# Optimization experiments

Hardware: AMD Instinct MI355X
Metric: run time of the kernel (lower is better)

## Reference

```python
import jax, jax.numpy as jnp
import numpy as np


def setup_inputs() -> dict:
    key = jax.random.key(0)
    k0, k1, k2, k3, k4 = jax.random.split(key, 5)
    B, S, D, E, H = 2, 4096, 1024, 8, 512
    x = jax.random.normal(k0, (B, S, D), jnp.float32)
    w_router = jax.random.normal(k1, (D, E), jnp.float32) * (D ** -0.5)
    w1 = jax.random.normal(k2, (E, D, H), jnp.float32) * (D ** -0.5)
    w2 = jax.random.normal(k3, (E, H, D), jnp.float32) * (H ** -0.5)
    w3 = jax.random.normal(k4, (E, D, H), jnp.float32) * (D ** -0.5)
    return {"x": x, "w_router": w_router, "w1": w1, "w2": w2, "w3": w3, "top_k": 2}


def reference(x, w_router, w1, w2, w3, top_k):
    """MoE layer: linear router -> softmax -> top_k, then grouped SwiGLU experts
    combined with the routing weights. out = sum_k w_k * Expert_{idx_k}(x)."""
    B, S, D = x.shape
    E = w_router.shape[1]
    xt = x.reshape(-1, D)                              # [T, D]
    T = xt.shape[0]

    # Router
    logits = xt @ w_router                             # [T, E]
    probs = jax.nn.softmax(logits, axis=-1)
    weights, idx = jax.lax.top_k(probs, top_k)         # [T, k], [T, k]

    # Scatter top-k weights into a dense per-token gate over experts.
    gate = jnp.zeros((T, E), xt.dtype).at[jnp.arange(T)[:, None], idx].add(weights)

    h = jax.nn.silu(jnp.einsum('td,edh->teh', xt, w1)) * jnp.einsum('td,edh->teh', xt, w3)
    y = jnp.einsum('te,teh,ehd->td', gate, h, w2)      # combine
    return y.reshape(B, S, D)
```

## Files before the change

kernel.cpp:

```cpp
#include <hip/hip_runtime.h>

#define NT    8192
#define DIM   1024
#define NE    8
#define NH    512
#define NROWS (NT*2)

typedef _Float16 f16;
typedef unsigned int u32;
typedef __attribute__((ext_vector_type(8))) _Float16 f16x8;
typedef __attribute__((ext_vector_type(4))) _Float16 f16x4;
typedef __attribute__((ext_vector_type(2))) _Float16 f16x2;
typedef __attribute__((ext_vector_type(4))) float f32x4;

__device__ __forceinline__ void gl2lds16(const f16* gptr, f16* ldsptr) {
    __builtin_amdgcn_global_load_lds(
        (const __attribute__((address_space(1))) u32*)gptr,
        (__attribute__((address_space(3))) u32*)ldsptr, 16, 0, 0);
}

#define FR(sbuf, row, q) \
    (*(const f16x8*)&sbuf[(row)*32 + (((q) ^ (((row) >> 1) & 3)) << 3)])

#define KC 512
__global__ __launch_bounds__(256) void prep_kernel(
    const float* __restrict__ x, const float* __restrict__ wr,
    const float* __restrict__ w1, const float* __restrict__ w3,
    const float* __restrict__ w2, float* __restrict__ plogits,
    f16* __restrict__ x16,
    f16* __restrict__ w1t, f16* __restrict__ w3t, f16* __restrict__ w2t,
    int* __restrict__ zint)
{
    __shared__ float smem[NE*KC];
    int tid = threadIdx.x;
    int bi = blockIdx.x;
    if (bi == 0 && tid < 16) zint[tid] = 0;
    if (bi < 1024) {
        int bx = bi & 511, by = bi >> 9;
        int kc0 = by * KC;
        for (int i = tid; i < NE*KC; i += 256) {
            int k = i >> 3, e = i & 7;
            smem[e*KC + k] = wr[(size_t)kc0*NE + i];
        }
        __syncthreads();
        int tok = bx*16 + (tid >> 4);
        int kl  = tid & 15;
        float acc[NE];
        #pragma unroll
        for (int e = 0; e < NE; e++) acc[e] = 0.f;
        const float* xrow = x + (size_t)tok*DIM + kc0;
        f16* xhrow = x16 + (size_t)tok*DIM + kc0;
        #pragma unroll
        for (int i = 0; i < KC/64; i++) {
            int kb = i*64 + kl*4;
            float4 xv = *(const float4*)(xrow + kb);
            f16x4 xh = { (f16)xv.x, (f16)xv.y, (f16)xv.z, (f16)xv.w };
            *(f16x4*)(xhrow + kb) = xh;
            #pragma unroll
            for (int e = 0; e < NE; e++) {
                float4 wv = *(const float4*)&smem[e*KC + kb];
                acc[e] += xv.x*wv.x + xv.y*wv.y + xv.z*wv.z + xv.w*wv.w;
            }
        }
        #pragma unroll
        for (int e = 0; e < NE; e++) {
            float v = acc[e];
            v += __shfl_xor(v, 1); v += __shfl_xor(v, 2);
            v += __shfl_xor(v, 4); v += __shfl_xor(v, 8);
            acc[e] = v;
        }
        if (kl == 0) {
            float* pp = plogits + ((size_t)by*NT + tok)*NE;
            float4 o0 = {acc[0], acc[1], acc[2], acc[3]};
            float4 o1 = {acc[4], acc[5], acc[6], acc[7]};
            *(float4*)pp = o0;
            *(float4*)(pp + 4) = o1;
        }
    } else {
        int tz = bi - 1024;
        int zx = tz & 127, zy = tz >> 7;
        int tensor = zy >> 3, e = zy & 7;
        const float* src; f16* dst; int R, C;
        if (tensor == 0)      { src = w1; dst = w1t; R = DIM; C = NH; }
        else if (tensor == 1) { src = w3; dst = w3t; R = DIM; C = NH; }
        else                  { src = w2; dst = w2t; R = NH; C = DIM; }
        src += (size_t)e * DIM * NH;
        dst += (size_t)e * DIM * NH;
        int tcols = C >> 6;
        int bx = zx % tcols, by = zx / tcols;
        int r0 = by*64, c0 = bx*64;
        #pragma unroll
        for (int p = 0; p < 4; p++) {
            int r = p*16 + (tid >> 4);
            int c = (tid & 15) << 2;
            float4 v = *(const float4*)&src[(size_t)(r0 + r)*C + c0 + c];
            *(float4*)&smem[r*64 + (c ^ (((r >> 3) & 7) << 2))] = v;
        }
        __syncthreads();
        #pragma unroll
        for (int pass = 0; pass < 2; pass++) {
            int s = pass*256 + tid;
            int h = s >> 3, a = s & 7, d0 = a << 3;
            int hs = h ^ (a << 2);
            f16x8 o;
            #pragma unroll
            for (int j = 0; j < 8; j++)
                o[j] = (f16)smem[(d0 + j)*64 + hs];
            *(f16x8*)&dst[(size_t)(c0 + h)*R + r0 + d0] = o;
        }
    }
}

__global__ __launch_bounds__(256) void route_kernel(
    const float* __restrict__ plogits, unsigned char* __restrict__ ge,
    float* __restrict__ gw, int* __restrict__ zint)
{
    __shared__ int lhist[NE];
    int tid = threadIdx.x;
    if (tid < NE) lhist[tid] = 0;
    __syncthreads();

    int t = blockIdx.x*256 + tid;
    const float* p0 = plogits + (size_t)t*NE;
    const float* p1 = plogits + (size_t)NT*NE + (size_t)t*NE;
    float4 a0 = *(const float4*)p0, a1 = *(const float4*)(p0+4);
    float4 b0 = *(const float4*)p1, b1 = *(const float4*)(p1+4);
    float l[NE] = { a0.x+b0.x, a0.y+b0.y, a0.z+b0.z, a0.w+b0.w,
                    a1.x+b1.x, a1.y+b1.y, a1.z+b1.z, a1.w+b1.w };
    float m = l[0];
    #pragma unroll
    for (int e = 1; e < NE; e++) m = fmaxf(m, l[e]);
    float s = 0.f;
    #pragma unroll
    for (int e = 0; e < NE; e++) { l[e] = __expf(l[e] - m); s += l[e]; }
    float inv = 1.f / s;
    int i0 = 0; float v0 = l[0];
    #pragma unroll
    for (int e = 1; e < NE; e++) if (l[e] > v0) { v0 = l[e]; i0 = e; }
    int i1 = -1; float v1 = -1.f;
    #pragma unroll
    for (int e = 0; e < NE; e++) if (e != i0 && l[e] > v1) { v1 = l[e]; i1 = e; }
    ge[2*t+0] = (unsigned char)i0; gw[2*t+0] = v0*inv;
    ge[2*t+1] = (unsigned char)i1; gw[2*t+1] = v1*inv;
    #pragma unroll
    for (int ee = 0; ee < NE; ee++) {
        int c = __popcll(__ballot(i0 == ee)) + __popcll(__ballot(i1 == ee));
        if ((tid & 63) == 0 && c) atomicAdd(&lhist[ee], c);
    }
    __syncthreads();
    if (tid < NE && lhist[tid]) atomicAdd(&zint[tid], lhist[tid]);
}

__global__ __launch_bounds__(256) void scatter_kernel(
    const unsigned char* __restrict__ ge, const float* __restrict__ gw,
    int* __restrict__ zint, int* __restrict__ offs, int* __restrict__ tok_ids,
    int* __restrict__ aid, float* __restrict__ row_gate)
{
    const int* ghist = zint;
    int* gcur = zint + 8;
    int tid = threadIdx.x;
    int loffs[NE]; int s = 0;
    #pragma unroll
    for (int e = 0; e < NE; e++) { loffs[e] = s; s += ghist[e]; }
    if (blockIdx.x == 0 && tid == 0) {
        #pragma unroll
        for (int e = 0; e < NE; e++) offs[e] = loffs[e];
        offs[NE] = s;
    }
    int id = blockIdx.x*256 + tid;
    int e = ge[id];
    float wv = gw[id];
    unsigned long long lt = (1ULL << (tid & 63)) - 1;
    int pos = 0;
    #pragma unroll
    for (int ee = 0; ee < NE; ee++) {
        unsigned long long mk = __ballot(e == ee);
        int cnt = __popcll(mk);
        int b = 0;
        if ((tid & 63) == 0 && cnt) b = atomicAdd(&gcur[ee], cnt);
        b = __shfl(b, 0);
        if (e == ee) pos = loffs[ee] + b + __popcll(mk & lt);
    }
    tok_ids[pos] = id >> 1;
    aid[pos] = id;
    row_gate[pos] = wv;
}


#define BM1 128
#define BN1 64
__global__ __launch_bounds__(256,3) void gemm1_kernel(
    const f16* __restrict__ x16, const int* __restrict__ tok_ids,
    const f16* __restrict__ w1t, const f16* __restrict__ w3t,
    f16* __restrict__ gbuf, const int* __restrict__ offs)
{
    int bi = blockIdx.x;
    int e  = bi & 7;
    int r_ = bi >> 3;
    int nt = r_ & 7;
    int mt = r_ >> 3;
    int off = offs[e];
    int n_e = offs[e+1] - off;
    if (mt*BM1 >= n_e) return;

    __shared__ f16 sA [2][BM1*32];
    __shared__ f16 sB1[2][BN1*32];
    __shared__ f16 sB3[2][BN1*32];
    __shared__ int stok[BM1];

    int tid = threadIdx.x;
    if (tid < BM1) {
        int rloc = mt*BM1 + tid; rloc = rloc < n_e ? rloc : n_e - 1;
        stok[tid] = tok_ids[off + rloc];
    }
    __syncthreads();

    int lane = tid & 63, w = tid >> 6;
    int wrow = (w >> 1)*64, wcol = (w & 1)*32;
    int q = lane >> 4, lm = lane & 15;

    int lr0 = w*32 + (lane >> 2);
    int lr1 = lr0 + 16;
    int gA0 = (lane & 3) ^ ((lr0 >> 1) & 3);
    int gA1 = (lane & 3) ^ ((lr1 >> 1) & 3);
    const f16* pA0 = x16 + (size_t)stok[lr0]*DIM + gA0*8;
    const f16* pA1 = x16 + (size_t)stok[lr1]*DIM + gA1*8;
    const int lofs0 = lr0*32 + ((lane & 3) << 3);
    const int lofs1 = lr1*32 + ((lane & 3) << 3);

    int br = w*16 + (lane >> 2);
    int gB = (lane & 3) ^ ((br >> 1) & 3);
    const f16* w1p = w1t + ((size_t)e*NH + nt*BN1)*DIM;
    const f16* w3p = w3t + ((size_t)e*NH + nt*BN1)*DIM;
    const f16* pb1 = w1p + (size_t)br*DIM + gB*8;
    const f16* pb3 = w3p + (size_t)br*DIM + gB*8;
    const int bofs = br*32 + ((lane & 3) << 3);

    f32x4 acc1[4][2], acc3[4][2];
    #pragma unroll
    for (int a = 0; a < 4; a++)
        #pragma unroll
        for (int b = 0; b < 2; b++) {
            acc1[a][b] = (f32x4){0.f,0.f,0.f,0.f};
            acc3[a][b] = (f32x4){0.f,0.f,0.f,0.f};
        }

    for (int k0 = 0; k0 < DIM; k0 += 64) {
        __syncthreads();
        gl2lds16(pA0 + k0,      &sA [0][lofs0]);
        gl2lds16(pA1 + k0,      &sA [0][lofs1]);
        gl2lds16(pA0 + k0 + 32, &sA [1][lofs0]);
        gl2lds16(pA1 + k0 + 32, &sA [1][lofs1]);
        gl2lds16(pb1 + k0,      &sB1[0][bofs]);
        gl2lds16(pb1 + k0 + 32, &sB1[1][bofs]);
        gl2lds16(pb3 + k0,      &sB3[0][bofs]);
        gl2lds16(pb3 + k0 + 32, &sB3[1][bofs]);
        __syncthreads();
        #pragma unroll
        for (int ks = 0; ks < 2; ks++) {
            f16x8 aF[4], b1F[2], b3F[2];
            #pragma unroll
            for (int s = 0; s < 4; s++) aF[s] = FR(sA[ks], wrow + s*16 + lm, q);
            #pragma unroll
            for (int c = 0; c < 2; c++) {
                b1F[c] = FR(sB1[ks], wcol + c*16 + lm, q);
                b3F[c] = FR(sB3[ks], wcol + c*16 + lm, q);
            }
            #pragma unroll
            for (int sr = 0; sr < 4; sr++)
                #pragma unroll
                for (int sc = 0; sc < 2; sc++) {
                    acc1[sr][sc] = __builtin_amdgcn_mfma_f32_16x16x32_f16(aF[sr], b1F[sc], acc1[sr][sc], 0, 0, 0);
                    acc3[sr][sc] = __builtin_amdgcn_mfma_f32_16x16x32_f16(aF[sr], b3F[sc], acc3[sr][sc], 0, 0, 0);
                }
        }
    }
    #pragma unroll
    for (int sr = 0; sr < 4; sr++) {
        #pragma unroll
        for (int reg = 0; reg < 4; reg++) {
            int row = mt*BM1 + wrow + sr*16 + q*4 + reg;
            if (row < n_e) {
                #pragma unroll
                for (int sc = 0; sc < 2; sc++) {
                    int col = nt*BN1 + wcol + sc*16 + lm;
                    float h1 = acc1[sr][sc][reg];
                    float h3 = acc3[sr][sc][reg];
                    float gv = h1 / (1.f + __expf(-h1)) * h3;
                    gbuf[(size_t)(off + row)*NH + col] = (f16)gv;
                }
            }
        }
    }
}

#define BM 128
#define BN 128
__global__ __launch_bounds__(256,3) void gemm2_kernel(
    const f16* __restrict__ gbuf, const f16* __restrict__ w2t,
    const int* __restrict__ offs, const int* __restrict__ aid,
    const float* __restrict__ row_gate, f16* __restrict__ ybuf)
{
    int bi = blockIdx.x;
    int e  = bi & 7;
    int r_ = bi >> 3;
    int nt = r_ & 7;
    int mt = r_ >> 3;
    int off = offs[e];
    int n_e = offs[e+1] - off;
    if (mt*BM >= n_e) return;

    __shared__ f16 sA[2][BM*32];
    __shared__ f16 sB[2][BN*32];
    __shared__ int said[BM];
    __shared__ float sgate[BM];

    int tid = threadIdx.x;
    if (tid < BM) {
        int rloc = mt*BM + tid;
        if (rloc < n_e) { said[tid] = aid[off + rloc]; sgate[tid] = row_gate[off + rloc]; }
        else            { said[tid] = 0; sgate[tid] = 0.f; }
    }

    int lane = tid & 63, w = tid >> 6;
    int wrow = (w >> 1)*64, wcol = (w & 1)*64;
    int q = lane >> 4, lm = lane & 15;

    int lr0 = w*32 + (lane >> 2);
    int lr1 = lr0 + 16;
    int g0 = (lane & 3) ^ ((lr0 >> 1) & 3);
    int g1 = (lane & 3) ^ ((lr1 >> 1) & 3);
    int ga0 = mt*BM + lr0; ga0 = ga0 < n_e ? ga0 : n_e - 1;
    int ga1 = mt*BM + lr1; ga1 = ga1 < n_e ? ga1 : n_e - 1;
    const f16* pA0 = gbuf + (size_t)(off + ga0)*NH + g0*8;
    const f16* pA1 = gbuf + (size_t)(off + ga1)*NH + g1*8;
    const f16* w2p = w2t + ((size_t)e*DIM + nt*BN)*NH;
    const f16* pB0 = w2p + (size_t)lr0*NH + g0*8;
    const f16* pB1 = w2p + (size_t)lr1*NH + g1*8;
    const int lofs0 = lr0*32 + ((lane & 3) << 3);
    const int lofs1 = lr1*32 + ((lane & 3) << 3);

    f32x4 acc[4][4];
    #pragma unroll
    for (int a = 0; a < 4; a++)
        #pragma unroll
        for (int b = 0; b < 4; b++) acc[a][b] = (f32x4){0.f,0.f,0.f,0.f};

    __syncthreads();

    for (int k0 = 0; k0 < NH; k0 += 64) {
        gl2lds16(pA0 + k0,      &sA[0][lofs0]);
        gl2lds16(pA1 + k0,      &sA[0][lofs1]);
        gl2lds16(pA0 + k0 + 32, &sA[1][lofs0]);
        gl2lds16(pA1 + k0 + 32, &sA[1][lofs1]);
        gl2lds16(pB0 + k0,      &sB[0][lofs0]);
        gl2lds16(pB1 + k0,      &sB[0][lofs1]);
        gl2lds16(pB0 + k0 + 32, &sB[1][lofs0]);
        gl2lds16(pB1 + k0 + 32, &sB[1][lofs1]);
        __syncthreads();
        #pragma unroll
        for (int ks = 0; ks < 2; ks++) {
            f16x8 aF[4], bF[4];
            #pragma unroll
            for (int s = 0; s < 4; s++) {
                aF[s] = FR(sA[ks], wrow + s*16 + lm, q);
                bF[s] = FR(sB[ks], wcol + s*16 + lm, q);
            }
            #pragma unroll
            for (int sr = 0; sr < 4; sr++)
                #pragma unroll
                for (int sc = 0; sc < 4; sc++)
                    acc[sr][sc] = __builtin_amdgcn_mfma_f32_16x16x32_f16(aF[sr], bF[sc], acc[sr][sc], 0, 0, 0);
        }
        __syncthreads();
    }
    #pragma unroll
    for (int sr = 0; sr < 4; sr++) {
        #pragma unroll
        for (int reg = 0; reg < 4; reg++) {
            int lrow = wrow + sr*16 + q*4 + reg;
            if (mt*BM + lrow < n_e) {
                int id = said[lrow];
                float wgt = sgate[lrow];
                #pragma unroll
                for (int sc = 0; sc < 4; sc++) {
                    int col = nt*BN + wcol + sc*16 + lm;
                    ybuf[(size_t)id*DIM + col] = (f16)(wgt * acc[sr][sc][reg]);
                }
            }
        }
    }
}

__global__ __launch_bounds__(256) void combine_kernel(
    const f16* __restrict__ ybuf, float* __restrict__ out)
{
    int gid = blockIdx.x*256 + threadIdx.x;
    int t = gid >> 7;
    int c = (gid & 127) << 3;
    f16x8 y0 = *(const f16x8*)(ybuf + ((size_t)2*t)*DIM + c);
    f16x8 y1 = *(const f16x8*)(ybuf + ((size_t)2*t+1)*DIM + c);
    float* op = out + (size_t)t*DIM + c;
    float4 o0 = { (float)y0[0] + (float)y1[0], (float)y0[1] + (float)y1[1],
                  (float)y0[2] + (float)y1[2], (float)y0[3] + (float)y1[3] };
    float4 o1 = { (float)y0[4] + (float)y1[4], (float)y0[5] + (float)y1[5],
                  (float)y0[6] + (float)y1[6], (float)y0[7] + (float)y1[7] };
    *(float4*)op = o0;
    *(float4*)(op + 4) = o1;
}

extern "C" void kernel_launch(void* const* d_in, const int* in_sizes, int n_in,
                              void* d_out, int out_size, void* d_ws, size_t ws_size,
                              hipStream_t stream)
{
    const float* x  = (const float*)d_in[0];
    const float* wr = (const float*)d_in[1];
    const float* w1 = (const float*)d_in[2];
    const float* w2 = (const float*)d_in[3];
    const float* w3 = (const float*)d_in[4];
    float* out = (float*)d_out;

    char* ws = (char*)d_ws;
    f16* ybuf    = (f16*)ws;        ws += (size_t)NROWS*DIM*sizeof(f16);
    f16* w1t     = (f16*)ws;        ws += (size_t)NE*NH*DIM*sizeof(f16);
    f16* w3t     = (f16*)ws;        ws += (size_t)NE*NH*DIM*sizeof(f16);
    f16* w2t     = (f16*)ws;        ws += (size_t)NE*DIM*NH*sizeof(f16);
    f16* gbuf    = (f16*)ws;        ws += (size_t)NROWS*NH*sizeof(f16);
    float* plogits = (float*)ws;    ws += (size_t)2*NT*NE*4;
    int* tok_ids = (int*)ws;        ws += (size_t)NROWS*4;
    int* aid     = (int*)ws;        ws += (size_t)NROWS*4;
    float* row_gate = (float*)ws;   ws += (size_t)NROWS*4;
    int* offs    = (int*)ws;        ws += 64;
    unsigned char* ge = (unsigned char*)ws; ws += (size_t)NROWS;
    float* gw    = (float*)ws;      ws += (size_t)NROWS*4;
    int* zint    = (int*)ws;        ws += 64;
    if (ws_size < (size_t)(ws - (char*)d_ws)) return;

    f16* x16 = ybuf;

    prep_kernel<<<1024 + 3072, 256, 0, stream>>>(x, wr, w1, w3, w2,
                                                 plogits, x16, w1t, w3t, w2t, zint);
    route_kernel<<<NT/256, 256, 0, stream>>>(plogits, ge, gw, zint);
    scatter_kernel<<<NROWS/256, 256, 0, stream>>>(ge, gw, zint, offs,
                                                  tok_ids, aid, row_gate);
    gemm1_kernel<<<4096, 256, 0, stream>>>(x16, tok_ids, w1t, w3t, gbuf, offs);
    gemm2_kernel<<<8192, 256, 0, stream>>>(gbuf, w2t, offs, aid, row_gate, ybuf);
    combine_kernel<<<(NT*(DIM/8))/256, 256, 0, stream>>>(ybuf, out);
}
```

Baseline: 238.6 us.

## Double-buffer gemm1 LDS staging and split prep into router and transpose kernels

The gemm1 k-loop now stages the next 64-wide K slice into a second LDS buffer while MFMAs run on the current one, leaving one barrier per iteration instead of two. This is meant to hide global-to-LDS latency. It doubles LDS use and lowers the occupancy hint from 3 to 2 blocks per CU. The fused prep kernel is also split into separate router and weight-transpose launches, which gives each smaller LDS footprints but adds one more launch.

New measurement: 257.5 us. 7.9% more time.

```diff
diff --git a/kernel.cpp b/kernel.cpp
--- a/kernel.cpp
+++ b/kernel.cpp
@@ -23,91 +23,94 @@
     (*(const f16x8*)&sbuf[(row)*32 + (((q) ^ (((row) >> 1) & 3)) << 3)])
 
 #define KC 512
-__global__ __launch_bounds__(256) void prep_kernel(
+__global__ __launch_bounds__(256) void prep_router_kernel(
     const float* __restrict__ x, const float* __restrict__ wr,
-    const float* __restrict__ w1, const float* __restrict__ w3,
-    const float* __restrict__ w2, float* __restrict__ plogits,
-    f16* __restrict__ x16,
-    f16* __restrict__ w1t, f16* __restrict__ w3t, f16* __restrict__ w2t,
+    float* __restrict__ plogits, f16* __restrict__ x16,
     int* __restrict__ zint)
 {
     __shared__ float smem[NE*KC];
     int tid = threadIdx.x;
     int bi = blockIdx.x;
     if (bi == 0 && tid < 16) zint[tid] = 0;
-    if (bi < 1024) {
-        int bx = bi & 511, by = bi >> 9;
-        int kc0 = by * KC;
-        for (int i = tid; i < NE*KC; i += 256) {
-            int k = i >> 3, e = i & 7;
-            smem[e*KC + k] = wr[(size_t)kc0*NE + i];
-        }
-        __syncthreads();
-        int tok = bx*16 + (tid >> 4);
-        int kl  = tid & 15;
-        float acc[NE];
-        #pragma unroll
-        for (int e = 0; e < NE; e++) acc[e] = 0.f;
-        const float* xrow = x + (size_t)tok*DIM + kc0;
-        f16* xhrow = x16 + (size_t)tok*DIM + kc0;
-        #pragma unroll
-        for (int i = 0; i < KC/64; i++) {
-            int kb = i*64 + kl*4;
-            float4 xv = *(const float4*)(xrow + kb);
-            f16x4 xh = { (f16)xv.x, (f16)xv.y, (f16)xv.z, (f16)xv.w };
-            *(f16x4*)(xhrow + kb) = xh;
-            #pragma unroll
-            for (int e = 0; e < NE; e++) {
-                float4 wv = *(const float4*)&smem[e*KC + kb];
-                acc[e] += xv.x*wv.x + xv.y*wv.y + xv.z*wv.z + xv.w*wv.w;
-            }
-        }
+    int bx = bi & 511, by = bi >> 9;
+    int kc0 = by * KC;
+    for (int i = tid; i < NE*KC; i += 256) {
+        int k = i >> 3, e = i & 7;
+        smem[e*KC + k] = wr[(size_t)kc0*NE + i];
+    }
+    __syncthreads();
+    int tok = bx*16 + (tid >> 4);
+    int kl  = tid & 15;
+    float acc[NE];
+    #pragma unroll
+    for (int e = 0; e < NE; e++) acc[e] = 0.f;
+    const float* xrow = x + (size_t)tok*DIM + kc0;
+    f16* xhrow = x16 + (size_t)tok*DIM + kc0;
+    #pragma unroll
+    for (int i = 0; i < KC/64; i++) {
+        int kb = i*64 + kl*4;
+        float4 xv = *(const float4*)(xrow + kb);
+        f16x4 xh = { (f16)xv.x, (f16)xv.y, (f16)xv.z, (f16)xv.w };
+        *(f16x4*)(xhrow + kb) = xh;
         #pragma unroll
         for (int e = 0; e < NE; e++) {
-            float v = acc[e];
-            v += __shfl_xor(v, 1); v += __shfl_xor(v, 2);
-            v += __shfl_xor(v, 4); v += __shfl_xor(v, 8);
-            acc[e] = v;
-        }
-        if (kl == 0) {
-            float* pp = plogits + ((size_t)by*NT + tok)*NE;
-            float4 o0 = {acc[0], acc[1], acc[2], acc[3]};
-            float4 o1 = {acc[4], acc[5], acc[6], acc[7]};
-            *(float4*)pp = o0;
-            *(float4*)(pp + 4) = o1;
-        }
-    } else {
-        int tz = bi - 1024;
-        int zx = tz & 127, zy = tz >> 7;
-        int tensor = zy >> 3, e = zy & 7;
-        const float* src; f16* dst; int R, C;
-        if (tensor == 0)      { src = w1; dst = w1t; R = DIM; C = NH; }
-        else if (tensor == 1) { src = w3; dst = w3t; R = DIM; C = NH; }
-        else                  { src = w2; dst = w2t; R = NH; C = DIM; }
-        src += (size_t)e * DIM * NH;
-        dst += (size_t)e * DIM * NH;
-        int tcols = C >> 6;
-        int bx = zx % tcols, by = zx / tcols;
-        int r0 = by*64, c0 = bx*64;
-        #pragma unroll
-        for (int p = 0; p < 4; p++) {
-            int r = p*16 + (tid >> 4);
-            int c = (tid & 15) << 2;
-            float4 v = *(const float4*)&src[(size_t)(r0 + r)*C + c0 + c];
-            *(float4*)&smem[r*64 + (c ^ (((r >> 3) & 7) << 2))] = v;
-        }
-        __syncthreads();
-        #pragma unroll
-        for (int pass = 0; pass < 2; pass++) {
-            int s = pass*256 + tid;
-            int h = s >> 3, a = s & 7, d0 = a << 3;
-            int hs = h ^ (a << 2);
-            f16x8 o;
-            #pragma unroll
-            for (int j = 0; j < 8; j++)
-                o[j] = (f16)smem[(d0 + j)*64 + hs];
-            *(f16x8*)&dst[(size_t)(c0 + h)*R + r0 + d0] = o;
-        }
+            float4 wv = *(const float4*)&smem[e*KC + kb];
+            acc[e] += xv.x*wv.x + xv.y*wv.y + xv.z*wv.z + xv.w*wv.w;
+        }
+    }
+    #pragma unroll
+    for (int e = 0; e < NE; e++) {
+        float v = acc[e];
+        v += __shfl_xor(v, 1); v += __shfl_xor(v, 2);
+        v += __shfl_xor(v, 4); v += __shfl_xor(v, 8);
+        acc[e] = v;
+    }
+    if (kl == 0) {
+        float* pp = plogits + ((size_t)by*NT + tok)*NE;
+        float4 o0 = {acc[0], acc[1], acc[2], acc[3]};
+        float4 o1 = {acc[4], acc[5], acc[6], acc[7]};
+        *(float4*)pp = o0;
+        *(float4*)(pp + 4) = o1;
+    }
+}
+
+__global__ __launch_bounds__(256) void prep_transpose_kernel(
+    const float* __restrict__ w1, const float* __restrict__ w3,
+    const float* __restrict__ w2,
+    f16* __restrict__ w1t, f16* __restrict__ w3t, f16* __restrict__ w2t)
+{
+    __shared__ float smem[64*64];
+    int tid = threadIdx.x;
+    int tz = blockIdx.x;
+    int zx = tz & 127, zy = tz >> 7;
+    int tensor = zy >> 3, e = zy & 7;
+    const float* src; f16* dst; int R, C;
+    if (tensor == 0)      { src = w1; dst = w1t; R = DIM; C = NH; }
+    else if (tensor == 1) { src = w3; dst = w3t; R = DIM; C = NH; }
+    else                  { src = w2; dst = w2t; R = NH; C = DIM; }
+    src += (size_t)e * DIM * NH;
+    dst += (size_t)e * DIM * NH;
+    int tcols = C >> 6;
+    int bx = zx % tcols, by = zx / tcols;
+    int r0 = by*64, c0 = bx*64;
+    #pragma unroll
+    for (int p = 0; p < 4; p++) {
+        int r = p*16 + (tid >> 4);
+        int c = (tid & 15) << 2;
+        float4 v = *(const float4*)&src[(size_t)(r0 + r)*C + c0 + c];
+        *(float4*)&smem[r*64 + (c ^ (((r >> 3) & 7) << 2))] = v;
+    }
+    __syncthreads();
+    #pragma unroll
+    for (int pass = 0; pass < 2; pass++) {
+        int s = pass*256 + tid;
+        int h = s >> 3, a = s & 7, d0 = a << 3;
+        int hs = h ^ (a << 2);
+        f16x8 o;
+        #pragma unroll
+        for (int j = 0; j < 8; j++)
+            o[j] = (f16)smem[(d0 + j)*64 + hs];
+        *(f16x8*)&dst[(size_t)(c0 + h)*R + r0 + d0] = o;
     }
 }
 
@@ -189,7 +192,7 @@
 
 #define BM1 128
 #define BN1 64
-__global__ __launch_bounds__(256,3) void gemm1_kernel(
+__global__ __launch_bounds__(256,2) void gemm1_kernel(
     const f16* __restrict__ x16, const int* __restrict__ tok_ids,
     const f16* __restrict__ w1t, const f16* __restrict__ w3t,
     f16* __restrict__ gbuf, const int* __restrict__ offs)
@@ -203,9 +206,9 @@
     int n_e = offs[e+1] - off;
     if (mt*BM1 >= n_e) return;
 
-    __shared__ f16 sA [2][BM1*32];
-    __shared__ f16 sB1[2][BN1*32];
-    __shared__ f16 sB3[2][BN1*32];
+    __shared__ f16 sA [2][2][BM1*32];
+    __shared__ f16 sB1[2][2][BN1*32];
+    __shared__ f16 sB3[2][2][BN1*32];
     __shared__ int stok[BM1];
 
     int tid = threadIdx.x;
@@ -245,26 +248,33 @@
             acc3[a][b] = (f32x4){0.f,0.f,0.f,0.f};
         }
 
-    for (int k0 = 0; k0 < DIM; k0 += 64) {
-        __syncthreads();
-        gl2lds16(pA0 + k0,      &sA [0][lofs0]);
-        gl2lds16(pA1 + k0,      &sA [0][lofs1]);
-        gl2lds16(pA0 + k0 + 32, &sA [1][lofs0]);
-        gl2lds16(pA1 + k0 + 32, &sA [1][lofs1]);
-        gl2lds16(pb1 + k0,      &sB1[0][bofs]);
-        gl2lds16(pb1 + k0 + 32, &sB1[1][bofs]);
-        gl2lds16(pb3 + k0,      &sB3[0][bofs]);
-        gl2lds16(pb3 + k0 + 32, &sB3[1][bofs]);
-        __syncthreads();
+    auto STAGE = [&](int b, int k0) {
+        gl2lds16(pA0 + k0,      &sA [b][0][lofs0]);
+        gl2lds16(pA1 + k0,      &sA [b][0][lofs1]);
+        gl2lds16(pA0 + k0 + 32, &sA [b][1][lofs0]);
+        gl2lds16(pA1 + k0 + 32, &sA [b][1][lofs1]);
+        gl2lds16(pb1 + k0,      &sB1[b][0][bofs]);
+        gl2lds16(pb1 + k0 + 32, &sB1[b][1][bofs]);
+        gl2lds16(pb3 + k0,      &sB3[b][0][bofs]);
+        gl2lds16(pb3 + k0 + 32, &sB3[b][1][bofs]);
+    };
+
+    STAGE(0, 0);
+    __syncthreads();
+
+    #pragma unroll 1
+    for (int t = 0; t < DIM/64; t++) {
+        int cur = t & 1;
+        if (t + 1 < DIM/64) STAGE(cur ^ 1, (t + 1)*64);
         #pragma unroll
         for (int ks = 0; ks < 2; ks++) {
             f16x8 aF[4], b1F[2], b3F[2];
             #pragma unroll
-            for (int s = 0; s < 4; s++) aF[s] = FR(sA[ks], wrow + s*16 + lm, q);
+            for (int s = 0; s < 4; s++) aF[s] = FR(sA[cur][ks], wrow + s*16 + lm, q);
             #pragma unroll
             for (int c = 0; c < 2; c++) {
-                b1F[c] = FR(sB1[ks], wcol + c*16 + lm, q);
-                b3F[c] = FR(sB3[ks], wcol + c*16 + lm, q);
+                b1F[c] = FR(sB1[cur][ks], wcol + c*16 + lm, q);
+                b3F[c] = FR(sB3[cur][ks], wcol + c*16 + lm, q);
             }
             #pragma unroll
             for (int sr = 0; sr < 4; sr++)
@@ -274,6 +284,7 @@
                     acc3[sr][sc] = __builtin_amdgcn_mfma_f32_16x16x32_f16(aF[sr], b3F[sc], acc3[sr][sc], 0, 0, 0);
                 }
         }
+        __syncthreads();
     }
     #pragma unroll
     for (int sr = 0; sr < 4; sr++) {
@@ -438,8 +449,8 @@
 
     f16* x16 = ybuf;
 
-    prep_kernel<<<1024 + 3072, 256, 0, stream>>>(x, wr, w1, w3, w2,
-                                                 plogits, x16, w1t, w3t, w2t, zint);
+    prep_router_kernel<<<1024, 256, 0, stream>>>(x, wr, plogits, x16, zint);
+    prep_transpose_kernel<<<3072, 256, 0, stream>>>(w1, w3, w2, w1t, w3t, w2t);
     route_kernel<<<NT/256, 256, 0, stream>>>(plogits, ge, gw, zint);
     scatter_kernel<<<NROWS/256, 256, 0, stream>>>(ge, gw, zint, offs,
                                                   tok_ids, aid, row_gate);
```

## Fuse routing softmax/top-k into prep kernel and use per-block histograms for scatter

Applied to the files above, without the earlier changes.

The router dot product now covers the full hidden dimension in each prep block, so softmax and top-2 selection run there directly. This removes the separate route kernel and the partial-logit buffer round trip. Expert counts are written as per-block histograms instead of global atomics, and the scatter kernel builds deterministic per-block prefix offsets from them, which also drops the need to zero a global counter. The trade-offs are a larger shared-memory router weight tile (32 KB), half as many routing blocks, and every scatter block redundantly re-reading all 512 histograms.

After: 221.0 us. -7.4%, faster.

```diff
diff --git a/kernel.cpp b/kernel.cpp
--- a/kernel.cpp
+++ b/kernel.cpp
@@ -5,6 +5,7 @@
 #define NE    8
 #define NH    512
 #define NROWS (NT*2)
+#define RTB   512
 
 typedef _Float16 f16;
 typedef unsigned int u32;
@@ -22,43 +23,42 @@
 #define FR(sbuf, row, q) \
     (*(const f16x8*)&sbuf[(row)*32 + (((q) ^ (((row) >> 1) & 3)) << 3)])
 
-#define KC 512
 __global__ __launch_bounds__(256) void prep_kernel(
     const float* __restrict__ x, const float* __restrict__ wr,
     const float* __restrict__ w1, const float* __restrict__ w3,
-    const float* __restrict__ w2, float* __restrict__ plogits,
+    const float* __restrict__ w2,
     f16* __restrict__ x16,
     f16* __restrict__ w1t, f16* __restrict__ w3t, f16* __restrict__ w2t,
-    int* __restrict__ zint)
-{
-    __shared__ float smem[NE*KC];
+    unsigned char* __restrict__ ge, float* __restrict__ gw,
+    int* __restrict__ bhist)
+{
+    __shared__ float smem[NE*DIM];
+    __shared__ int lhist[NE];
     int tid = threadIdx.x;
     int bi = blockIdx.x;
-    if (bi == 0 && tid < 16) zint[tid] = 0;
-    if (bi < 1024) {
-        int bx = bi & 511, by = bi >> 9;
-        int kc0 = by * KC;
-        for (int i = tid; i < NE*KC; i += 256) {
+    if (bi < RTB) {
+        if (tid < NE) lhist[tid] = 0;
+        for (int i = tid; i < NE*DIM; i += 256) {
             int k = i >> 3, e = i & 7;
-            smem[e*KC + k] = wr[(size_t)kc0*NE + i];
-        }
-        __syncthreads();
-        int tok = bx*16 + (tid >> 4);
+            smem[e*DIM + k] = wr[i];
+        }
+        __syncthreads();
+        int tok = bi*16 + (tid >> 4);
         int kl  = tid & 15;
         float acc[NE];
         #pragma unroll
         for (int e = 0; e < NE; e++) acc[e] = 0.f;
-        const float* xrow = x + (size_t)tok*DIM + kc0;
-        f16* xhrow = x16 + (size_t)tok*DIM + kc0;
-        #pragma unroll
-        for (int i = 0; i < KC/64; i++) {
+        const float* xrow = x + (size_t)tok*DIM;
+        f16* xhrow = x16 + (size_t)tok*DIM;
+        #pragma unroll
+        for (int i = 0; i < DIM/64; i++) {
             int kb = i*64 + kl*4;
             float4 xv = *(const float4*)(xrow + kb);
             f16x4 xh = { (f16)xv.x, (f16)xv.y, (f16)xv.z, (f16)xv.w };
             *(f16x4*)(xhrow + kb) = xh;
             #pragma unroll
             for (int e = 0; e < NE; e++) {
-                float4 wv = *(const float4*)&smem[e*KC + kb];
+                float4 wv = *(const float4*)&smem[e*DIM + kb];
                 acc[e] += xv.x*wv.x + xv.y*wv.y + xv.z*wv.z + xv.w*wv.w;
             }
         }
@@ -69,15 +69,33 @@
             v += __shfl_xor(v, 4); v += __shfl_xor(v, 8);
             acc[e] = v;
         }
+        float m = acc[0];
+        #pragma unroll
+        for (int e = 1; e < NE; e++) m = fmaxf(m, acc[e]);
+        float s = 0.f;
+        #pragma unroll
+        for (int e = 0; e < NE; e++) { acc[e] = __expf(acc[e] - m); s += acc[e]; }
+        float inv = 1.f / s;
+        int i0 = 0; float v0 = acc[0];
+        #pragma unroll
+        for (int e = 1; e < NE; e++) if (acc[e] > v0) { v0 = acc[e]; i0 = e; }
+        int i1 = -1; float v1 = -1.f;
+        #pragma unroll
+        for (int e = 0; e < NE; e++) if (e != i0 && acc[e] > v1) { v1 = acc[e]; i1 = e; }
         if (kl == 0) {
-            float* pp = plogits + ((size_t)by*NT + tok)*NE;
-            float4 o0 = {acc[0], acc[1], acc[2], acc[3]};
-            float4 o1 = {acc[4], acc[5], acc[6], acc[7]};
-            *(float4*)pp = o0;
-            *(float4*)(pp + 4) = o1;
-        }
+            ge[2*tok+0] = (unsigned char)i0; gw[2*tok+0] = v0*inv;
+            ge[2*tok+1] = (unsigned char)i1; gw[2*tok+1] = v1*inv;
+        }
+        #pragma unroll
+        for (int ee = 0; ee < NE; ee++) {
+            int c = __popcll(__ballot(kl == 0 && i0 == ee))
+                  + __popcll(__ballot(kl == 0 && i1 == ee));
+            if ((tid & 63) == 0 && c) atomicAdd(&lhist[ee], c);
+        }
+        __syncthreads();
+        if (tid < NE) bhist[(size_t)bi*NE + tid] = lhist[tid];
     } else {
-        int tz = bi - 1024;
+        int tz = bi - RTB;
         int zx = tz & 127, zy = tz >> 7;
         int tensor = zy >> 3, e = zy & 7;
         const float* src; f16* dst; int R, C;
@@ -111,75 +129,59 @@
     }
 }
 
-__global__ __launch_bounds__(256) void route_kernel(
-    const float* __restrict__ plogits, unsigned char* __restrict__ ge,
-    float* __restrict__ gw, int* __restrict__ zint)
-{
-    __shared__ int lhist[NE];
-    int tid = threadIdx.x;
-    if (tid < NE) lhist[tid] = 0;
-    __syncthreads();
-
-    int t = blockIdx.x*256 + tid;
-    const float* p0 = plogits + (size_t)t*NE;
-    const float* p1 = plogits + (size_t)NT*NE + (size_t)t*NE;
-    float4 a0 = *(const float4*)p0, a1 = *(const float4*)(p0+4);
-    float4 b0 = *(const float4*)p1, b1 = *(const float4*)(p1+4);
-    float l[NE] = { a0.x+b0.x, a0.y+b0.y, a0.z+b0.z, a0.w+b0.w,
-                    a1.x+b1.x, a1.y+b1.y, a1.z+b1.z, a1.w+b1.w };
-    float m = l[0];
-    #pragma unroll
-    for (int e = 1; e < NE; e++) m = fmaxf(m, l[e]);
-    float s = 0.f;
-    #pragma unroll
-    for (int e = 0; e < NE; e++) { l[e] = __expf(l[e] - m); s += l[e]; }
-    float inv = 1.f / s;
-    int i0 = 0; float v0 = l[0];
-    #pragma unroll
-    for (int e = 1; e < NE; e++) if (l[e] > v0) { v0 = l[e]; i0 = e; }
-    int i1 = -1; float v1 = -1.f;
-    #pragma unroll
-    for (int e = 0; e < NE; e++) if (e != i0 && l[e] > v1) { v1 = l[e]; i1 = e; }
-    ge[2*t+0] = (unsigned char)i0; gw[2*t+0] = v0*inv;
-    ge[2*t+1] = (unsigned char)i1; gw[2*t+1] = v1*inv;
-    #pragma unroll
-    for (int ee = 0; ee < NE; ee++) {
-        int c = __popcll(__ballot(i0 == ee)) + __popcll(__ballot(i1 == ee));
-        if ((tid & 63) == 0 && c) atomicAdd(&lhist[ee], c);
-    }
-    __syncthreads();
-    if (tid < NE && lhist[tid]) atomicAdd(&zint[tid], lhist[tid]);
-}
-
 __global__ __launch_bounds__(256) void scatter_kernel(
     const unsigned char* __restrict__ ge, const float* __restrict__ gw,
-    int* __restrict__ zint, int* __restrict__ offs, int* __restrict__ tok_ids,
-    int* __restrict__ aid, float* __restrict__ row_gate)
-{
-    const int* ghist = zint;
-    int* gcur = zint + 8;
+    const int* __restrict__ bhist, int* __restrict__ offs,
+    int* __restrict__ tok_ids, int* __restrict__ aid,
+    float* __restrict__ row_gate)
+{
+    __shared__ int part_tot[32][NE], part_pre[32][NE];
+    __shared__ int s_tot[NE], cur[NE];
     int tid = threadIdx.x;
+    int bi = blockIdx.x;
+
+    int e = tid & 7, c = tid >> 3;
+    int lim = bi*8;
+    int tot = 0, pre = 0;
+    for (int b = c; b < RTB; b += 32) {
+        int v = bhist[(size_t)b*NE + e];
+        tot += v;
+        if (b < lim) pre += v;
+    }
+    part_tot[c][e] = tot; part_pre[c][e] = pre;
+    __syncthreads();
+    if (tid < NE) {
+        int t2 = 0, p2 = 0;
+        #pragma unroll
+        for (int c2 = 0; c2 < 32; c2++) { t2 += part_tot[c2][tid]; p2 += part_pre[c2][tid]; }
+        s_tot[tid] = t2;
+        part_pre[0][tid] = p2;
+    }
+    __syncthreads();
     int loffs[NE]; int s = 0;
     #pragma unroll
-    for (int e = 0; e < NE; e++) { loffs[e] = s; s += ghist[e]; }
-    if (blockIdx.x == 0 && tid == 0) {
-        #pragma unroll
-        for (int e = 0; e < NE; e++) offs[e] = loffs[e];
+    for (int ee = 0; ee < NE; ee++) { loffs[ee] = s; s += s_tot[ee]; }
+    if (bi == 0 && tid == 0) {
+        #pragma unroll
+        for (int ee = 0; ee < NE; ee++) offs[ee] = loffs[ee];
         offs[NE] = s;
     }
-    int id = blockIdx.x*256 + tid;
-    int e = ge[id];
+    if (tid < NE) cur[tid] = loffs[tid] + part_pre[0][tid];
+    __syncthreads();
+
+    int id = bi*256 + tid;
+    int my_e = ge[id];
     float wv = gw[id];
     unsigned long long lt = (1ULL << (tid & 63)) - 1;
     int pos = 0;
     #pragma unroll
     for (int ee = 0; ee < NE; ee++) {
-        unsigned long long mk = __ballot(e == ee);
+        unsigned long long mk = __ballot(my_e == ee);
         int cnt = __popcll(mk);
         int b = 0;
-        if ((tid & 63) == 0 && cnt) b = atomicAdd(&gcur[ee], cnt);
+        if ((tid & 63) == 0 && cnt) b = atomicAdd(&cur[ee], cnt);
         b = __shfl(b, 0);
-        if (e == ee) pos = loffs[ee] + b + __popcll(mk & lt);
+        if (my_e == ee) pos = b + __popcll(mk & lt);
     }
     tok_ids[pos] = id >> 1;
     aid[pos] = id;
@@ -426,22 +428,21 @@
     f16* w3t     = (f16*)ws;        ws += (size_t)NE*NH*DIM*sizeof(f16);
     f16* w2t     = (f16*)ws;        ws += (size_t)NE*DIM*NH*sizeof(f16);
     f16* gbuf    = (f16*)ws;        ws += (size_t)NROWS*NH*sizeof(f16);
-    float* plogits = (float*)ws;    ws += (size_t)2*NT*NE*4;
     int* tok_ids = (int*)ws;        ws += (size_t)NROWS*4;
     int* aid     = (int*)ws;        ws += (size_t)NROWS*4;
     float* row_gate = (float*)ws;   ws += (size_t)NROWS*4;
     int* offs    = (int*)ws;        ws += 64;
     unsigned char* ge = (unsigned char*)ws; ws += (size_t)NROWS;
     float* gw    = (float*)ws;      ws += (size_t)NROWS*4;
-    int* zint    = (int*)ws;        ws += 64;
+    int* bhist   = (int*)ws;        ws += (size_t)RTB*NE*4;
     if (ws_size < (size_t)(ws - (char*)d_ws)) return;
 
     f16* x16 = ybuf;
 
-    prep_kernel<<<1024 + 3072, 256, 0, stream>>>(x, wr, w1, w3, w2,
-                                                 plogits, x16, w1t, w3t, w2t, zint);
-    route_kernel<<<NT/256, 256, 0, stream>>>(plogits, ge, gw, zint);
-    scatter_kernel<<<NROWS/256, 256, 0, stream>>>(ge, gw, zint, offs,
+    prep_kernel<<<RTB + 3072, 256, 0, stream>>>(x, wr, w1, w3, w2,
+                                                x16, w1t, w3t, w2t,
+                                                ge, gw, bhist);
+    scatter_kernel<<<NROWS/256, 256, 0, stream>>>(ge, gw, bhist, offs,
                                                   tok_ids, aid, row_gate);
     gemm1_kernel<<<4096, 256, 0, stream>>>(x16, tok_ids, w1t, w3t, gbuf, offs);
     gemm2_kernel<<<8192, 256, 0, stream>>>(gbuf, w2t, offs, aid, row_gate, ybuf);
```
